# Optimization experiments

Hardware: AMD Instinct MI355X
Metric: run time of the kernel (lower is better)

The kernel has to match this reference:

```python
import jax, jax.numpy as jnp
import numpy as np

BATCH = 2048
DIM = 100000
K = 16


def setup_inputs() -> dict:
    key = jax.random.key(0)
    k1, k2, k3 = jax.random.split(key, 3)
    inputs = jax.random.uniform(k1, (BATCH, DIM), dtype=jnp.float32)
    w = jax.random.normal(k2, (DIM, 1), dtype=jnp.float32)
    v = jax.random.normal(k3, (DIM, K), dtype=jnp.float32)
    return {"inputs": inputs, "w": w, "v": v}


def reference(inputs, w, v):
    # linear term: [batch]
    logits = jnp.squeeze(inputs @ w, axis=-1)
    # 2nd-order FM interaction via square-of-sum minus sum-of-square trick
    square_of_sum = jnp.square(inputs @ v)              # [batch, k]
    sum_of_square = jnp.square(inputs) @ jnp.square(v)  # [batch, k]
    logits = logits + 0.5 * jnp.sum(square_of_sum - sum_of_square, axis=1)
    return logits
```

## Files before the change

### kernel.cpp

```cpp
#include <hip/hip_runtime.h>
#include <hip/hip_bf16.h>

#define BATCH 2048
#define DIM   100000
#define STEPS 3125
#define NSPLIT 8
#define NTILES 25
#define ROWTILES 128

typedef float f32x4  __attribute__((ext_vector_type(4)));
typedef short bf16x8 __attribute__((ext_vector_type(8)));
typedef short bf16x4 __attribute__((ext_vector_type(4)));

__device__ __forceinline__ short f2bf(float f) {
    return (short)__builtin_bit_cast(unsigned short, __float2bfloat16(f));
}
__device__ __forceinline__ float bf2f(short s) {
    unsigned u = ((unsigned)(unsigned short)s) << 16;
    return __builtin_bit_cast(float, u);
}

__global__ __launch_bounds__(256) void fm_pack(
        const float* __restrict__ w, const float* __restrict__ v,
        short* __restrict__ Bv, short* __restrict__ Bc) {
    __shared__ float vt[128][17];
    __shared__ float wt[128];
    const int t  = threadIdx.x;
    const int jb = blockIdx.x * 4;
    const int d_base = jb * 32;
    const int nd = (DIM - d_base < 128) ? (DIM - d_base) : 128;

    #pragma unroll
    for (int q = 0; q < 2; ++q) {
        int e = t * 8 + q * 4;
        if (e < nd * 16) {
            f32x4 r = *(const f32x4*)(v + (size_t)d_base * 16 + e);
            #pragma unroll
            for (int i = 0; i < 4; ++i) vt[(e + i) >> 4][(e + i) & 15] = r[i];
        }
    }
    if (t < 32) {
        int d = t * 4;
        if (d < nd) {
            f32x4 r = *(const f32x4*)(w + d_base + d);
            #pragma unroll
            for (int i = 0; i < 4; ++i) if (d + i < nd) wt[d + i] = r[i];
        }
    }
    __syncthreads();

    const int jp = t >> 6;
    const int j  = jb + jp;
    if (j >= STEPS) return;
    const int rem = t & 63;
    const int h = rem >> 4, c = rem & 15;
    const int dl0 = jp * 32 + h * 8;
    size_t off = (size_t)j * 512 + h * 128 + c * 8;

    bf16x8 ov, oc;
    #pragma unroll
    for (int i = 0; i < 8; ++i) ov[i] = f2bf(vt[dl0 + i][c]);
    *(bf16x8*)(Bv + off) = ov;

    if (c == 0) {
        #pragma unroll
        for (int i = 0; i < 8; ++i) oc[i] = f2bf(wt[dl0 + i]);
    } else if (c == 1) {
        #pragma unroll
        for (int i = 0; i < 8; ++i) {
            float s = 0.f;
            #pragma unroll
            for (int k = 0; k < 16; ++k) { float vv = vt[dl0 + i][k]; s += vv * vv; }
            oc[i] = f2bf(s);
        }
    } else {
        oc = (bf16x8)0;
    }
    *(bf16x8*)(Bc + off) = oc;
}

__global__ __launch_bounds__(256, 4) void fm_main(
        const float* __restrict__ x,
        const short* __restrict__ Bv, const short* __restrict__ Bc,
        float* __restrict__ P) {
    const int bid     = blockIdx.x;
    const int split   = bid & 7;
    const int rowtile = bid >> 3;
    const int lane = threadIdx.x & 63;
    const int wave = threadIdx.x >> 6;
    const int c = lane & 15;
    const int h = lane >> 4;

    const int step_base  = split * 390 + (split < 5 ? split : 5);
    const int tail_steps = 6 + (split < 5 ? 1 : 0);

    __shared__ short lds[2][16 * 512];

    const int col0s = step_base * 32;
    f32x4 st[4][2];
    bf16x8 bvr[4], bcr[4];

    f32x4 acc_s = {0.f, 0.f, 0.f, 0.f};
    f32x4 acc_l = {0.f, 0.f, 0.f, 0.f};
    f32x4 acc_q = {0.f, 0.f, 0.f, 0.f};

    auto issue = [&](int t) {
        if (t >= NTILES) return;
        const int ncols = (t < 24) ? 512 : tail_steps * 32;
        const int colf = col0s + t * 512;
        #pragma unroll
        for (int R = 0; R < 4; ++R) {
            int r = wave * 4 + R;
            const float* p = x + (size_t)(rowtile * 16 + r) * DIM + colf;
            if (lane * 4 < ncols)
                st[R][0] = __builtin_nontemporal_load((const f32x4*)(p + lane * 4));
            if (256 + lane * 4 < ncols)
                st[R][1] = __builtin_nontemporal_load((const f32x4*)(p + 256 + lane * 4));
        }
    };
    auto writeLDS = [&](int buf, int t) {
        if (t >= NTILES) return;
        const int ncols = (t < 24) ? 512 : tail_steps * 32;
        #pragma unroll
        for (int R = 0; R < 4; ++R) {
            int r = wave * 4 + R;
            int swz = (r & 7) << 4;
            char* base = (char*)&lds[buf][0];
            if (lane * 4 < ncols) {
                bf16x4 o; 
                #pragma unroll
                for (int i = 0; i < 4; ++i) o[i] = f2bf(st[R][0][i]);
                *(bf16x4*)(base + (r * 1024 + ((lane * 8) ^ swz))) = o;
            }
            if (256 + lane * 4 < ncols) {
                bf16x4 o;
                #pragma unroll
                for (int i = 0; i < 4; ++i) o[i] = f2bf(st[R][1][i]);
                *(bf16x4*)(base + (r * 1024 + ((512 + lane * 8) ^ swz))) = o;
            }
        }
    };
    auto loadB = [&](int t) {
        if (t >= NTILES) return;
        int jbase = step_base + t * 16;
        #pragma unroll
        for (int ss = 0; ss < 4; ++ss) {
            int s = jbase + wave * 4 + ss;
            if (s > STEPS - 1) s = STEPS - 1;
            size_t off = (size_t)s * 512 + h * 128 + c * 8;
            bvr[ss] = *(const bf16x8*)(Bv + off);
            bcr[ss] = *(const bf16x8*)(Bc + off);
        }
    };
    auto compute = [&](int buf, int t) {
        const int nsteps = (t < 24) ? 16 : tail_steps;
        const char* base = (const char*)&lds[buf][0];
        const int swz = (c & 7) << 4;
        #pragma unroll
        for (int ss = 0; ss < 4; ++ss) {
            int s = wave * 4 + ss;
            if (s < nsteps) {
                bf16x8 a1 = *(const bf16x8*)(base + (c * 1024 + ((s * 64 + h * 16) ^ swz)));
                bf16x8 a2;
                #pragma unroll
                for (int i = 0; i < 8; ++i) {
                    float f = bf2f(a1[i]);
                    a2[i] = f2bf(f * f);
                }
                acc_s = __builtin_amdgcn_mfma_f32_16x16x32_bf16(a1, bvr[ss], acc_s, 0, 0, 0);
                acc_l = __builtin_amdgcn_mfma_f32_16x16x32_bf16(a1, bcr[ss], acc_l, 0, 0, 0);
                acc_q = __builtin_amdgcn_mfma_f32_16x16x32_bf16(a2, bcr[ss], acc_q, 0, 0, 0);
            }
        }
    };

    loadB(0);
    issue(0);
    writeLDS(0, 0);
    issue(1);
    for (int t = 0; t < NTILES; ++t) {
        __syncthreads();
        compute(t & 1, t);
        loadB(t + 1);
        writeLDS((t + 1) & 1, t + 1);
        issue(t + 2);
    }

    __syncthreads();
    float* red = (float*)&lds[0][0];
    int rbase = (wave * 64 + lane) * 12;
    #pragma unroll
    for (int i = 0; i < 4; ++i) {
        red[rbase + i]     = acc_s[i];
        red[rbase + 4 + i] = acc_l[i];
        red[rbase + 8 + i] = acc_q[i];
    }
    __syncthreads();
    if (wave == 0) {
        f32x4 s = {0,0,0,0}, l = {0,0,0,0}, q = {0,0,0,0};
        #pragma unroll
        for (int wv = 0; wv < 4; ++wv) {
            const float* rp = &red[(wv * 64 + lane) * 12];
            #pragma unroll
            for (int i = 0; i < 4; ++i) {
                s[i] += rp[i]; l[i] += rp[4 + i]; q[i] += rp[8 + i];
            }
        }
        #pragma unroll
        for (int r = 0; r < 4; ++r) {
            size_t row = (size_t)rowtile * 16 + h * 4 + r;
            float* Pp = P + (row * NSPLIT + split) * 18;
            Pp[c] = s[r];
            if (c == 0) Pp[16] = l[r];
            if (c == 1) Pp[17] = q[r];
        }
    }
}

__global__ __launch_bounds__(64) void fm_reduce(const float* __restrict__ P,
                                                float* __restrict__ out) {
    int b = blockIdx.x;
    int lane = threadIdx.x;
    float r[18];
    if (lane < NSPLIT) {
        const float* q = P + ((size_t)b * NSPLIT + lane) * 18;
        #pragma unroll
        for (int i = 0; i < 18; ++i) r[i] = q[i];
    } else {
        #pragma unroll
        for (int i = 0; i < 18; ++i) r[i] = 0.f;
    }
    #pragma unroll
    for (int off = 4; off > 0; off >>= 1) {
        #pragma unroll
        for (int i = 0; i < 18; ++i) r[i] += __shfl_xor(r[i], off, 64);
    }
    if (lane == 0) {
        float acc = r[16] - 0.5f * r[17];
        #pragma unroll
        for (int k = 0; k < 16; ++k) acc += 0.5f * r[k] * r[k];
        out[b] = acc;
    }
}

extern "C" void kernel_launch(void* const* d_in, const int* in_sizes, int n_in,
                              void* d_out, int out_size, void* d_ws, size_t ws_size,
                              hipStream_t stream) {
    const float* x = (const float*)d_in[0];
    const float* w = (const float*)d_in[1];
    const float* v = (const float*)d_in[2];
    float* out = (float*)d_out;

    char* ws = (char*)d_ws;
    short* Bv = (short*)(ws);
    short* Bc = (short*)(ws + 3200000);
    float* P  = (float*)(ws + 6400000);

    fm_pack<<<(STEPS + 3) / 4, 256, 0, stream>>>(w, v, Bv, Bc);
    fm_main<<<NSPLIT * ROWTILES, 256, 0, stream>>>(x, Bv, Bc, P);
    fm_reduce<<<BATCH, 64, 0, stream>>>(P, out);
}
```

Measured before the change: 158.5 us.

## Split reduction dimension 32 ways with single-wave blocks and no barriers

Reworks the main kernel so each block is a single 64-thread wave. The reduction dimension is split 32 ways instead of 8, and each tile covers 128 columns with 4 MFMA steps. This removes __syncthreads and the LDS cross-wave reduction: each wave writes its partials straight to the workspace, and the reduce kernel shuffles across 32 splits. In exchange, there are four times as many partial rows, each row now reads shorter contiguous 512-byte runs, and prefetch depth drops from two tiles ahead to one.

```diff
diff --git a/kernel.cpp b/kernel.cpp
--- a/kernel.cpp
+++ b/kernel.cpp
@@ -4,7 +4,7 @@
 #define BATCH 2048
 #define DIM   100000
 #define STEPS 3125
-#define NSPLIT 8
+#define NSPLIT 32
 #define NTILES 25
 #define ROWTILES 128
 
@@ -79,25 +79,26 @@
     *(bf16x8*)(Bc + off) = oc;
 }
 
-__global__ __launch_bounds__(256, 4) void fm_main(
+__global__ __launch_bounds__(64, 4) void fm_main(
         const float* __restrict__ x,
         const short* __restrict__ Bv, const short* __restrict__ Bc,
         float* __restrict__ P) {
     const int bid     = blockIdx.x;
-    const int split   = bid & 7;
-    const int rowtile = bid >> 3;
-    const int lane = threadIdx.x & 63;
-    const int wave = threadIdx.x >> 6;
+    const int split   = bid & 31;
+    const int rowtile = bid >> 5;
+    const int lane = threadIdx.x;
     const int c = lane & 15;
     const int h = lane >> 4;
 
-    const int step_base  = split * 390 + (split < 5 ? split : 5);
-    const int tail_steps = 6 + (split < 5 ? 1 : 0);
-
-    __shared__ short lds[2][16 * 512];
+    const int step_base  = split * 97 + (split < 21 ? split : 21);
+    const int tail_steps = (split < 21) ? 2 : 1;
+
+    __shared__ short lds[2][16 * 128];
 
     const int col0s = step_base * 32;
-    f32x4 st[4][2];
+    const int lrow2 = lane >> 5;
+    const int lcol  = (lane & 31) * 4;
+    f32x4 st[8];
     bf16x8 bvr[4], bcr[4];
 
     f32x4 acc_s = {0.f, 0.f, 0.f, 0.f};
@@ -106,46 +107,39 @@
 
     auto issue = [&](int t) {
         if (t >= NTILES) return;
-        const int ncols = (t < 24) ? 512 : tail_steps * 32;
-        const int colf = col0s + t * 512;
-        #pragma unroll
-        for (int R = 0; R < 4; ++R) {
-            int r = wave * 4 + R;
+        const int ncols = (t < 24) ? 128 : tail_steps * 32;
+        const bool ok = lcol < ncols;
+        const int colf = col0s + t * 128 + lcol;
+        #pragma unroll
+        for (int L = 0; L < 8; ++L) {
+            int r = L * 2 + lrow2;
             const float* p = x + (size_t)(rowtile * 16 + r) * DIM + colf;
-            if (lane * 4 < ncols)
-                st[R][0] = __builtin_nontemporal_load((const f32x4*)(p + lane * 4));
-            if (256 + lane * 4 < ncols)
-                st[R][1] = __builtin_nontemporal_load((const f32x4*)(p + 256 + lane * 4));
+            if (ok) st[L] = __builtin_nontemporal_load((const f32x4*)p);
         }
     };
     auto writeLDS = [&](int buf, int t) {
         if (t >= NTILES) return;
-        const int ncols = (t < 24) ? 512 : tail_steps * 32;
-        #pragma unroll
-        for (int R = 0; R < 4; ++R) {
-            int r = wave * 4 + R;
-            int swz = (r & 7) << 4;
-            char* base = (char*)&lds[buf][0];
-            if (lane * 4 < ncols) {
-                bf16x4 o; 
-                #pragma unroll
-                for (int i = 0; i < 4; ++i) o[i] = f2bf(st[R][0][i]);
-                *(bf16x4*)(base + (r * 1024 + ((lane * 8) ^ swz))) = o;
-            }
-            if (256 + lane * 4 < ncols) {
+        const int ncols = (t < 24) ? 128 : tail_steps * 32;
+        const bool ok = lcol < ncols;
+        char* base = (char*)&lds[buf][0];
+        #pragma unroll
+        for (int L = 0; L < 8; ++L) {
+            int r = L * 2 + lrow2;
+            int byte = r * 256 + ((lcol * 2) ^ ((r & 7) << 4));
+            if (ok) {
                 bf16x4 o;
                 #pragma unroll
-                for (int i = 0; i < 4; ++i) o[i] = f2bf(st[R][1][i]);
-                *(bf16x4*)(base + (r * 1024 + ((512 + lane * 8) ^ swz))) = o;
+                for (int i = 0; i < 4; ++i) o[i] = f2bf(st[L][i]);
+                *(bf16x4*)(base + byte) = o;
             }
         }
     };
     auto loadB = [&](int t) {
         if (t >= NTILES) return;
-        int jbase = step_base + t * 16;
+        int jbase = step_base + t * 4;
         #pragma unroll
         for (int ss = 0; ss < 4; ++ss) {
-            int s = jbase + wave * 4 + ss;
+            int s = jbase + ss;
             if (s > STEPS - 1) s = STEPS - 1;
             size_t off = (size_t)s * 512 + h * 128 + c * 8;
             bvr[ss] = *(const bf16x8*)(Bv + off);
@@ -153,14 +147,13 @@
         }
     };
     auto compute = [&](int buf, int t) {
-        const int nsteps = (t < 24) ? 16 : tail_steps;
+        const int nsteps = (t < 24) ? 4 : tail_steps;
         const char* base = (const char*)&lds[buf][0];
         const int swz = (c & 7) << 4;
         #pragma unroll
         for (int ss = 0; ss < 4; ++ss) {
-            int s = wave * 4 + ss;
-            if (s < nsteps) {
-                bf16x8 a1 = *(const bf16x8*)(base + (c * 1024 + ((s * 64 + h * 16) ^ swz)));
+            if (ss < nsteps) {
+                bf16x8 a1 = *(const bf16x8*)(base + (c * 256 + ((ss * 64 + h * 16) ^ swz)));
                 bf16x8 a2;
                 #pragma unroll
                 for (int i = 0; i < 8; ++i) {
@@ -174,46 +167,21 @@
         }
     };
 
-    loadB(0);
     issue(0);
-    writeLDS(0, 0);
-    issue(1);
     for (int t = 0; t < NTILES; ++t) {
-        __syncthreads();
+        loadB(t);
+        writeLDS(t & 1, t);
+        issue(t + 1);
         compute(t & 1, t);
-        loadB(t + 1);
-        writeLDS((t + 1) & 1, t + 1);
-        issue(t + 2);
-    }
-
-    __syncthreads();
-    float* red = (float*)&lds[0][0];
-    int rbase = (wave * 64 + lane) * 12;
-    #pragma unroll
-    for (int i = 0; i < 4; ++i) {
-        red[rbase + i]     = acc_s[i];
-        red[rbase + 4 + i] = acc_l[i];
-        red[rbase + 8 + i] = acc_q[i];
-    }
-    __syncthreads();
-    if (wave == 0) {
-        f32x4 s = {0,0,0,0}, l = {0,0,0,0}, q = {0,0,0,0};
-        #pragma unroll
-        for (int wv = 0; wv < 4; ++wv) {
-            const float* rp = &red[(wv * 64 + lane) * 12];
-            #pragma unroll
-            for (int i = 0; i < 4; ++i) {
-                s[i] += rp[i]; l[i] += rp[4 + i]; q[i] += rp[8 + i];
-            }
-        }
-        #pragma unroll
-        for (int r = 0; r < 4; ++r) {
-            size_t row = (size_t)rowtile * 16 + h * 4 + r;
-            float* Pp = P + (row * NSPLIT + split) * 18;
-            Pp[c] = s[r];
-            if (c == 0) Pp[16] = l[r];
-            if (c == 1) Pp[17] = q[r];
-        }
+    }
+
+    #pragma unroll
+    for (int r = 0; r < 4; ++r) {
+        size_t row = (size_t)rowtile * 16 + h * 4 + r;
+        float* Pp = P + (row * NSPLIT + split) * 18;
+        Pp[c] = acc_s[r];
+        if (c == 0) Pp[16] = acc_l[r];
+        if (c == 1) Pp[17] = acc_q[r];
     }
 }
 
@@ -231,7 +199,7 @@
         for (int i = 0; i < 18; ++i) r[i] = 0.f;
     }
     #pragma unroll
-    for (int off = 4; off > 0; off >>= 1) {
+    for (int off = 16; off > 0; off >>= 1) {
         #pragma unroll
         for (int i = 0; i < 18; ++i) r[i] += __shfl_xor(r[i], off, 64);
     }
@@ -257,6 +225,6 @@
     float* P  = (float*)(ws + 6400000);
 
     fm_pack<<<(STEPS + 3) / 4, 256, 0, stream>>>(w, v, Bv, Bc);
-    fm_main<<<NSPLIT * ROWTILES, 256, 0, stream>>>(x, Bv, Bc, P);
+    fm_main<<<NSPLIT * ROWTILES, 64, 0, stream>>>(x, Bv, Bc, P);
     fm_reduce<<<BATCH, 64, 0, stream>>>(P, out);
 }
```

Measured after the change: 178.8 us. 12.8% more time.
